# Performance work log

Hardware: AMD Instinct MI355X
Metric: run time of the kernel (lower is better)

Reference implementation:

```python
import jax, jax.numpy as jnp
import numpy as np

B, S, D = 4, 2048, 1024
E, K, H = 8, 2, 4096


def setup_inputs() -> dict:
    key = jax.random.key(0)
    ks = jax.random.split(key, 8)
    sd = 1.0 / np.sqrt(D)
    sh = 1.0 / np.sqrt(H)
    x = jax.random.normal(ks[0], (B, S, D), dtype=jnp.float32)
    gate_w = jax.random.normal(ks[1], (D, E), dtype=jnp.float32) * sd
    gate_b = jnp.zeros((E,), dtype=jnp.float32)
    w1 = jax.random.normal(ks[2], (E, D, H), dtype=jnp.float32) * sd
    b1 = jnp.zeros((E, H), dtype=jnp.float32)
    w2 = jax.random.normal(ks[3], (E, H, D), dtype=jnp.float32) * sh
    b2 = jnp.zeros((E, D), dtype=jnp.float32)
    return {"x": x, "gate_w": gate_w, "gate_b": gate_b,
            "w1": w1, "b1": b1, "w2": w2, "b2": b2}


def reference(x, gate_w, gate_b, w1, b1, w2, b2):
    # gate logits [B,S,E]
    logits = jnp.einsum('bsd,de->bse', x, gate_w) + gate_b
    # top-k over experts, softmax over the k selected (dim=2), in float32
    weights, selected = jax.lax.top_k(logits, K)            # [B,S,K]
    weights = jax.nn.softmax(weights.astype(jnp.float32), axis=-1).astype(x.dtype)
    out = jnp.zeros_like(x)
    for i in range(E):
        # per-token combine weight for expert i (0 if not routed here)
        w_i = jnp.sum(jnp.where(selected == i, weights, 0.0), axis=-1)  # [B,S]
        h = jax.nn.gelu(jnp.einsum('bsd,dh->bsh', x, w1[i]) + b1[i])    # [B,S,H]
        y = jnp.einsum('bsh,hd->bsd', h, w2[i]) + b2[i]                  # [B,S,D]
        out = out + w_i[..., None] * y
    return out
```

## Files before the change

### kernel.cpp

```cpp
#include <hip/hip_runtime.h>
#include <hip/hip_bf16.h>
#include <stdint.h>

#define T_TOK 8192
#define D_DIM 1024
#define E_NUM 8
#define H_DIM 4096
#define NPAD 144
#define PPX (NPAD / 8)
#define GATEB 2048
#define TRB 4096

typedef short bf16x8 __attribute__((ext_vector_type(8)));
typedef float f32x4 __attribute__((ext_vector_type(4)));
typedef unsigned short usv8 __attribute__((ext_vector_type(8)));

#define AS1 __attribute__((address_space(1)))
#define AS3 __attribute__((address_space(3)))

__device__ __forceinline__ unsigned short f2b(float f) {
  union { float f; uint32_t u; } v; v.f = f;
  uint32_t r = (v.u + 0x7fffu + ((v.u >> 16) & 1u)) >> 16;
  return (unsigned short)r;
}

__device__ __forceinline__ float gelu_tanh(float x) {
  float u = 0.7978845608028654f * (x + 0.044715f * x * x * x);
  u = fminf(fmaxf(u, -15.f), 15.f);
  float e = __expf(2.f * u);
  float t = (e - 1.f) / (e + 1.f);
  return 0.5f * x * (1.f + t);
}

__device__ __forceinline__ void gload_lds16(const void* g, void* l) {
  __builtin_amdgcn_global_load_lds((const AS1 uint32_t*)g, (AS3 uint32_t*)l, 16, 0, 0);
}

__global__ __launch_bounds__(256) void moe_prep(const float* __restrict__ x,
                                                const float* __restrict__ gw,
                                                const float* __restrict__ gb,
                                                const float* __restrict__ w1,
                                                const float* __restrict__ w2,
                                                const float* __restrict__ b2,
                                                unsigned short* __restrict__ xb,
                                                unsigned short* __restrict__ w1t,
                                                unsigned short* __restrict__ w2t,
                                                int2* __restrict__ sel,
                                                float2* __restrict__ wts,
                                                int* __restrict__ meta,
                                                float* __restrict__ out) {
  __shared__ unsigned short tile[64][260];
  int z = blockIdx.x;
  if (z >= GATEB) {
    int z2 = z - GATEB;
    int e = (z2 >> 8) & 7;
    int bx = z2 & 255;
    const float* in; unsigned short* outp; int R, C, ry, cy;
    if (z2 < TRB / 2) { in = w1 + (size_t)e * D_DIM * H_DIM; outp = w1t + (size_t)e * D_DIM * H_DIM;
                        R = D_DIM; C = H_DIM; ry = bx >> 6; cy = bx & 63; }
    else              { in = w2 + (size_t)e * H_DIM * D_DIM; outp = w2t + (size_t)e * H_DIM * D_DIM;
                        R = H_DIM; C = D_DIM; ry = bx >> 4; cy = bx & 15; }
    int r0 = ry * 256, c0 = cy * 64;
    int t = threadIdx.x;
    int sc = (t & 15) * 4;
    int srb = (t >> 4) * 4;
#pragma unroll
    for (int it = 0; it < 4; ++it) {
      int sr = srb + it * 64;
      float4 v0 = *(const float4*)(in + (size_t)(r0 + sr + 0) * C + c0 + sc);
      float4 v1 = *(const float4*)(in + (size_t)(r0 + sr + 1) * C + c0 + sc);
      float4 v2 = *(const float4*)(in + (size_t)(r0 + sr + 2) * C + c0 + sc);
      float4 v3 = *(const float4*)(in + (size_t)(r0 + sr + 3) * C + c0 + sc);
      ushort4 o;
      o.x = f2b(v0.x); o.y = f2b(v1.x); o.z = f2b(v2.x); o.w = f2b(v3.x);
      *(ushort4*)&tile[sc + 0][sr] = o;
      o.x = f2b(v0.y); o.y = f2b(v1.y); o.z = f2b(v2.y); o.w = f2b(v3.y);
      *(ushort4*)&tile[sc + 1][sr] = o;
      o.x = f2b(v0.z); o.y = f2b(v1.z); o.z = f2b(v2.z); o.w = f2b(v3.z);
      *(ushort4*)&tile[sc + 2][sr] = o;
      o.x = f2b(v0.w); o.y = f2b(v1.w); o.z = f2b(v2.w); o.w = f2b(v3.w);
      *(ushort4*)&tile[sc + 3][sr] = o;
    }
    __syncthreads();
    int wv = t >> 6, lane = t & 63;
    int rowHalf = lane >> 5, el = (lane & 31) * 8;
#pragma unroll
    for (int it = 0; it < 8; ++it) {
      int orow = wv * 16 + it * 2 + rowHalf;
      usv8 o = *(const usv8*)&tile[orow][el];
      *(usv8*)(outp + (size_t)(c0 + orow) * R + r0 + el) = o;
    }
    return;
  }
  int lane = threadIdx.x & 63;
  int t = z * 4 + (threadIdx.x >> 6);
  const float* xr = x + (size_t)t * D_DIM;
  unsigned short* xo = xb + (size_t)t * D_DIM;
  float acc[8];
#pragma unroll
  for (int e = 0; e < 8; e++) acc[e] = 0.f;
#pragma unroll
  for (int i = 0; i < 4; i++) {
    int d0 = lane * 4 + i * 256;
    float4 xv = *(const float4*)(xr + d0);
    ushort4 o;
    o.x = f2b(xv.x); o.y = f2b(xv.y); o.z = f2b(xv.z); o.w = f2b(xv.w);
    *(ushort4*)(xo + d0) = o;
    const float* gp = gw + (size_t)d0 * 8;
    float xs[4] = {xv.x, xv.y, xv.z, xv.w};
#pragma unroll
    for (int j = 0; j < 4; j++) {
#pragma unroll
      for (int e = 0; e < 8; e++) acc[e] += xs[j] * gp[j * 8 + e];
    }
  }
#pragma unroll
  for (int off = 32; off > 0; off >>= 1) {
#pragma unroll
    for (int e = 0; e < 8; e++) acc[e] += __shfl_xor(acc[e], off);
  }
  float lg[8];
#pragma unroll
  for (int e = 0; e < 8; e++) lg[e] = acc[e] + gb[e];
  int e0 = 0; float b0v = lg[0];
#pragma unroll
  for (int e = 1; e < 8; e++) if (lg[e] > b0v) { b0v = lg[e]; e0 = e; }
  int e1 = -1; float b1v = -1e30f;
#pragma unroll
  for (int e = 0; e < 8; e++) if (e != e0 && lg[e] > b1v) { b1v = lg[e]; e1 = e; }
  float d = __expf(b1v - b0v);
  float w0 = 1.f / (1.f + d), w1v = d / (1.f + d);
  if (lane == 0) {
    sel[t] = make_int2(e0, e1);
    wts[t] = make_float2(w0, w1v);
    atomicAdd(&meta[e0], 1);
    atomicAdd(&meta[e1], 1);
  }
  const float* ba = b2 + (size_t)e0 * D_DIM;
  const float* bb = b2 + (size_t)e1 * D_DIM;
  float* orow = out + (size_t)t * D_DIM;
#pragma unroll
  for (int k = 0; k < 4; k++) {
    int dd = lane * 4 + k * 256;
    float4 a = *(const float4*)(ba + dd);
    float4 b = *(const float4*)(bb + dd);
    float4 o;
    o.x = w0 * a.x + w1v * b.x;
    o.y = w0 * a.y + w1v * b.y;
    o.z = w0 * a.z + w1v * b.z;
    o.w = w0 * a.w + w1v * b.w;
    *(float4*)(orow + dd) = o;
  }
}

__global__ __launch_bounds__(256) void moe_scatter(const int2* __restrict__ sel,
                                                   const float2* __restrict__ wts,
                                                   int* __restrict__ meta,
                                                   int* __restrict__ token_id,
                                                   float* __restrict__ weightv) {
  int t = blockIdx.x * 256 + threadIdx.x;
  if (t >= T_TOK) return;
  int cnt[8];
#pragma unroll
  for (int e = 0; e < 8; e++) cnt[e] = meta[e];
  int2 s = sel[t];
  float2 w = wts[t];
  int o0 = 0, o1 = 0;
#pragma unroll
  for (int e = 0; e < 8; e++) {
    if (e < s.x) o0 += cnt[e];
    if (e < s.y) o1 += cnt[e];
  }
  int p0 = o0 + atomicAdd(&meta[20 + s.x], 1); token_id[p0] = t; weightv[p0] = w.x;
  int p1 = o1 + atomicAdd(&meta[20 + s.y], 1); token_id[p1] = t; weightv[p1] = w.y;
}

__device__ __forceinline__ bool panel_decode(const int* __restrict__ meta, int wi,
                                             int& e, int& m0, int& seg, int& ne) {
  int acc = 0, pre = 0;
  e = -1;
#pragma unroll
  for (int k = 0; k < 8; k++) {
    int ck = meta[k];
    int nb = (ck + 127) >> 7;
    if (wi >= acc && wi < acc + nb) { e = k; m0 = (wi - acc) << 7; seg = pre; ne = ck; }
    acc += nb; pre += ck;
  }
  return e >= 0;
}


__global__ __launch_bounds__(256, 4) void moe_gemm1(const unsigned short* __restrict__ xb,
                                                    const unsigned short* __restrict__ w1t,
                                                    const float* __restrict__ b1,
                                                    const int* __restrict__ meta,
                                                    const int* __restrict__ token_id,
                                                    unsigned short* __restrict__ hbuf) {
  int b = blockIdx.x;
  int c = b & 7, u = b >> 3;
  int n = u & 31, ps = u >> 5;
  int e, m0, seg, ne;
  if (!panel_decode(meta, c * PPX + ps, e, m0, seg, ne)) return;
  int n0 = n * 128;
  const unsigned short* wB = w1t + (size_t)e * H_DIM * D_DIM;

  __shared__ unsigned short As[2][4096];
  __shared__ unsigned short Bs[2][4096];

  int tid = threadIdx.x, lane = tid & 63, wv = tid >> 6;
  const unsigned short* aptr[2];
  const unsigned short* bptr[2];
#pragma unroll
  for (int q = 0; q < 2; q++) {
    int chunk = tid + q * 256;
    int row = chunk >> 2;
    int ko = ((chunk & 3) ^ ((chunk >> 3) & 3)) * 8;
    int gi = m0 + row; if (gi >= ne) gi = m0;
    int tok = token_id[seg + gi];
    aptr[q] = xb + (size_t)tok * D_DIM + ko;
    bptr[q] = wB + (size_t)(n0 + row) * D_DIM + ko;
  }
  auto stage = [&](int buf, int kt) {
#pragma unroll
    for (int q = 0; q < 2; q++) {
      gload_lds16(aptr[q] + kt * 32, &As[buf][(wv + 4 * q) * 512]);
      gload_lds16(bptr[q] + kt * 32, &Bs[buf][(wv + 4 * q) * 512]);
    }
  };

  f32x4 acc[4][4] = {};
  int wr = wv >> 1, wc = wv & 1;
  int sswz = ((lane >> 4) ^ ((lane >> 1) & 3)) * 8;
  int abase = (wr * 64 + (lane & 15)) * 32 + sswz;
  int bbase = (wc * 64 + (lane & 15)) * 32 + sswz;

  stage(0, 0);
  __syncthreads();
  const int nk = D_DIM / 32;
  for (int kt = 0; kt < nk; ++kt) {
    int cur = kt & 1;
    if (kt + 1 < nk) stage(cur ^ 1, kt + 1);
    bf16x8 af[4], bfr[4];
#pragma unroll
    for (int m = 0; m < 4; m++) af[m] = *(const bf16x8*)&As[cur][abase + m * 512];
#pragma unroll
    for (int nn = 0; nn < 4; nn++) bfr[nn] = *(const bf16x8*)&Bs[cur][bbase + nn * 512];
#pragma unroll
    for (int m = 0; m < 4; m++)
#pragma unroll
      for (int nn = 0; nn < 4; nn++)
        acc[m][nn] = __builtin_amdgcn_mfma_f32_16x16x32_bf16(af[m], bfr[nn], acc[m][nn], 0, 0, 0);
    __syncthreads();
  }

  int rbase = wr * 64 + (lane >> 4) * 4;
  int cbase = n0 + wc * 64 + (lane & 15);
  const float* b1e = b1 + (size_t)e * H_DIM + cbase;
  float bv[4];
#pragma unroll
  for (int nn = 0; nn < 4; nn++) bv[nn] = b1e[nn * 16];
#pragma unroll
  for (int m = 0; m < 4; m++) {
#pragma unroll
    for (int j = 0; j < 4; j++) {
      int gi = m0 + rbase + m * 16 + j;
      if (gi < ne) {
        unsigned short* hrow = hbuf + (size_t)(seg + gi) * H_DIM + cbase;
#pragma unroll
        for (int nn = 0; nn < 4; nn++) {
          float v = acc[m][nn][j] + bv[nn];
          hrow[nn * 16] = f2b(gelu_tanh(v));
        }
      }
    }
  }
}

__global__ __launch_bounds__(256, 4) void moe_gemm2(const unsigned short* __restrict__ hbuf,
                                                    const unsigned short* __restrict__ w2t,
                                                    const int* __restrict__ meta,
                                                    const int* __restrict__ token_id,
                                                    const float* __restrict__ weightv,
                                                    float* __restrict__ out) {
  int b = blockIdx.x;
  int c = b & 7, u = b >> 3;
  int n = u & 7, ks = (u >> 3) & 1, ps = u >> 4;
  int e, m0, seg, ne;
  if (!panel_decode(meta, c * PPX + ps, e, m0, seg, ne)) return;
  int n0 = n * 128;
  int kbase = ks * 2048;
  const unsigned short* wB = w2t + (size_t)e * D_DIM * H_DIM;

  __shared__ unsigned short As[2][4096];
  __shared__ unsigned short Bs[2][4096];

  int tid = threadIdx.x, lane = tid & 63, wv = tid >> 6;
  const unsigned short* aptr[2];
  const unsigned short* bptr[2];
#pragma unroll
  for (int q = 0; q < 2; q++) {
    int chunk = tid + q * 256;
    int row = chunk >> 2;
    int ko = ((chunk & 3) ^ ((chunk >> 3) & 3)) * 8;
    int gi = m0 + row; if (gi >= ne) gi = m0;
    aptr[q] = hbuf + (size_t)(seg + gi) * H_DIM + kbase + ko;
    bptr[q] = wB + (size_t)(n0 + row) * H_DIM + kbase + ko;
  }
  auto stage = [&](int buf, int kt) {
#pragma unroll
    for (int q = 0; q < 2; q++) {
      gload_lds16(aptr[q] + kt * 32, &As[buf][(wv + 4 * q) * 512]);
      gload_lds16(bptr[q] + kt * 32, &Bs[buf][(wv + 4 * q) * 512]);
    }
  };

  f32x4 acc[4][4] = {};
  int wr = wv >> 1, wc = wv & 1;
  int sswz = ((lane >> 4) ^ ((lane >> 1) & 3)) * 8;
  int abase = (wr * 64 + (lane & 15)) * 32 + sswz;
  int bbase = (wc * 64 + (lane & 15)) * 32 + sswz;

  stage(0, 0);
  __syncthreads();
  const int nk = 2048 / 32;
  for (int kt = 0; kt < nk; ++kt) {
    int cur = kt & 1;
    if (kt + 1 < nk) stage(cur ^ 1, kt + 1);
    bf16x8 af[4], bfr[4];
#pragma unroll
    for (int m = 0; m < 4; m++) af[m] = *(const bf16x8*)&As[cur][abase + m * 512];
#pragma unroll
    for (int nn = 0; nn < 4; nn++) bfr[nn] = *(const bf16x8*)&Bs[cur][bbase + nn * 512];
#pragma unroll
    for (int m = 0; m < 4; m++)
#pragma unroll
      for (int nn = 0; nn < 4; nn++)
        acc[m][nn] = __builtin_amdgcn_mfma_f32_16x16x32_bf16(af[m], bfr[nn], acc[m][nn], 0, 0, 0);
    __syncthreads();
  }

  int rbase = wr * 64 + (lane >> 4) * 4;
  int cbase = n0 + wc * 64 + (lane & 15);
#pragma unroll
  for (int m = 0; m < 4; m++) {
#pragma unroll
    for (int j = 0; j < 4; j++) {
      int gi = m0 + rbase + m * 16 + j;
      if (gi < ne) {
        int p = seg + gi;
        int tok = token_id[p];
        float wt = weightv[p];
        float* orow = out + (size_t)tok * D_DIM + cbase;
#pragma unroll
        for (int nn = 0; nn < 4; nn++)
          atomicAdd(&orow[nn * 16], wt * acc[m][nn][j]);
      }
    }
  }
}

extern "C" void kernel_launch(void* const* d_in, const int* in_sizes, int n_in,
                              void* d_out, int out_size, void* d_ws, size_t ws_size,
                              hipStream_t stream) {
  const float* x      = (const float*)d_in[0];
  const float* gate_w = (const float*)d_in[1];
  const float* gate_b = (const float*)d_in[2];
  const float* w1     = (const float*)d_in[3];
  const float* b1     = (const float*)d_in[4];
  const float* w2     = (const float*)d_in[5];
  const float* b2     = (const float*)d_in[6];
  float* out = (float*)d_out;

  uint8_t* ws = (uint8_t*)d_ws;
  unsigned short* hbuf = (unsigned short*)(ws);
  unsigned short* xb   = (unsigned short*)(ws + 134217728ull);
  unsigned short* w1t  = (unsigned short*)(ws + 150994944ull);
  unsigned short* w2t  = (unsigned short*)(ws + 218103808ull);
  int*    token_id = (int*)  (ws + 285212672ull);
  float*  weightv  = (float*)(ws + 285278208ull);
  float2* wts      = (float2*)(ws + 285343744ull);
  int2*   sel      = (int2*) (ws + 285409280ull);
  int*    meta     = (int*)  (ws + 285474816ull);

  hipMemsetAsync(meta, 0, 128, stream);

  moe_prep<<<dim3(GATEB + TRB), 256, 0, stream>>>(
      x, gate_w, gate_b, w1, w2, b2, xb, w1t, w2t, sel, wts, meta, out);
  moe_scatter<<<dim3(T_TOK / 256), 256, 0, stream>>>(sel, wts, meta, token_id, weightv);

  moe_gemm1<<<dim3(NPAD * 32), 256, 0, stream>>>(xb, w1t, b1, meta, token_id, hbuf);
  moe_gemm2<<<dim3(NPAD * 16), 256, 0, stream>>>(hbuf, w2t, meta, token_id, weightv, out);
}
```

Measured before the change: 795.9 us.

## Move w2 transpose into gemm1 launch to overlap with expert GEMM

Splits the weight transpose work so only w1 is converted in the prep kernel. The w2 fp32-to-bf16 transpose now runs as extra leading blocks in the gemm1 launch, sharing its LDS buffer (sized to fit the 64x260 tile). The aim is to shorten the prep kernel's critical path and overlap w2 conversion with the first GEMM's compute. In exchange, gemm1's shared memory allocation grows, which may reduce occupancy, and the transpose blocks compete with GEMM blocks for bandwidth and CUs.

```diff
diff --git a/kernel.cpp b/kernel.cpp
--- a/kernel.cpp
+++ b/kernel.cpp
@@ -9,7 +9,8 @@
 #define NPAD 144
 #define PPX (NPAD / 8)
 #define GATEB 2048
-#define TRB 4096
+#define TRB1 2048
+#define TRB2 2048
 
 typedef short bf16x8 __attribute__((ext_vector_type(8)));
 typedef float f32x4 __attribute__((ext_vector_type(4)));
@@ -36,15 +37,47 @@
   __builtin_amdgcn_global_load_lds((const AS1 uint32_t*)g, (AS3 uint32_t*)l, 16, 0, 0);
 }
 
+__device__ __forceinline__ void transpose_tile(const float* __restrict__ in,
+                                               unsigned short* __restrict__ outp,
+                                               int R, int C, int r0, int c0,
+                                               unsigned short (*tile)[260], int t) {
+  int sc = (t & 15) * 4;
+  int srb = (t >> 4) * 4;
+#pragma unroll
+  for (int it = 0; it < 4; ++it) {
+    int sr = srb + it * 64;
+    float4 v0 = *(const float4*)(in + (size_t)(r0 + sr + 0) * C + c0 + sc);
+    float4 v1 = *(const float4*)(in + (size_t)(r0 + sr + 1) * C + c0 + sc);
+    float4 v2 = *(const float4*)(in + (size_t)(r0 + sr + 2) * C + c0 + sc);
+    float4 v3 = *(const float4*)(in + (size_t)(r0 + sr + 3) * C + c0 + sc);
+    ushort4 o;
+    o.x = f2b(v0.x); o.y = f2b(v1.x); o.z = f2b(v2.x); o.w = f2b(v3.x);
+    *(ushort4*)&tile[sc + 0][sr] = o;
+    o.x = f2b(v0.y); o.y = f2b(v1.y); o.z = f2b(v2.y); o.w = f2b(v3.y);
+    *(ushort4*)&tile[sc + 1][sr] = o;
+    o.x = f2b(v0.z); o.y = f2b(v1.z); o.z = f2b(v2.z); o.w = f2b(v3.z);
+    *(ushort4*)&tile[sc + 2][sr] = o;
+    o.x = f2b(v0.w); o.y = f2b(v1.w); o.z = f2b(v2.w); o.w = f2b(v3.w);
+    *(ushort4*)&tile[sc + 3][sr] = o;
+  }
+  __syncthreads();
+  int wv = t >> 6, lane = t & 63;
+  int rowHalf = lane >> 5, el = (lane & 31) * 8;
+#pragma unroll
+  for (int it = 0; it < 8; ++it) {
+    int orow = wv * 16 + it * 2 + rowHalf;
+    usv8 o = *(const usv8*)&tile[orow][el];
+    *(usv8*)(outp + (size_t)(c0 + orow) * R + r0 + el) = o;
+  }
+}
+
 __global__ __launch_bounds__(256) void moe_prep(const float* __restrict__ x,
                                                 const float* __restrict__ gw,
                                                 const float* __restrict__ gb,
                                                 const float* __restrict__ w1,
-                                                const float* __restrict__ w2,
                                                 const float* __restrict__ b2,
                                                 unsigned short* __restrict__ xb,
                                                 unsigned short* __restrict__ w1t,
-                                                unsigned short* __restrict__ w2t,
                                                 int2* __restrict__ sel,
                                                 float2* __restrict__ wts,
                                                 int* __restrict__ meta,
@@ -53,43 +86,9 @@
   int z = blockIdx.x;
   if (z >= GATEB) {
     int z2 = z - GATEB;
-    int e = (z2 >> 8) & 7;
-    int bx = z2 & 255;
-    const float* in; unsigned short* outp; int R, C, ry, cy;
-    if (z2 < TRB / 2) { in = w1 + (size_t)e * D_DIM * H_DIM; outp = w1t + (size_t)e * D_DIM * H_DIM;
-                        R = D_DIM; C = H_DIM; ry = bx >> 6; cy = bx & 63; }
-    else              { in = w2 + (size_t)e * H_DIM * D_DIM; outp = w2t + (size_t)e * H_DIM * D_DIM;
-                        R = H_DIM; C = D_DIM; ry = bx >> 4; cy = bx & 15; }
-    int r0 = ry * 256, c0 = cy * 64;
-    int t = threadIdx.x;
-    int sc = (t & 15) * 4;
-    int srb = (t >> 4) * 4;
-#pragma unroll
-    for (int it = 0; it < 4; ++it) {
-      int sr = srb + it * 64;
-      float4 v0 = *(const float4*)(in + (size_t)(r0 + sr + 0) * C + c0 + sc);
-      float4 v1 = *(const float4*)(in + (size_t)(r0 + sr + 1) * C + c0 + sc);
-      float4 v2 = *(const float4*)(in + (size_t)(r0 + sr + 2) * C + c0 + sc);
-      float4 v3 = *(const float4*)(in + (size_t)(r0 + sr + 3) * C + c0 + sc);
-      ushort4 o;
-      o.x = f2b(v0.x); o.y = f2b(v1.x); o.z = f2b(v2.x); o.w = f2b(v3.x);
-      *(ushort4*)&tile[sc + 0][sr] = o;
-      o.x = f2b(v0.y); o.y = f2b(v1.y); o.z = f2b(v2.y); o.w = f2b(v3.y);
-      *(ushort4*)&tile[sc + 1][sr] = o;
-      o.x = f2b(v0.z); o.y = f2b(v1.z); o.z = f2b(v2.z); o.w = f2b(v3.z);
-      *(ushort4*)&tile[sc + 2][sr] = o;
-      o.x = f2b(v0.w); o.y = f2b(v1.w); o.z = f2b(v2.w); o.w = f2b(v3.w);
-      *(ushort4*)&tile[sc + 3][sr] = o;
-    }
-    __syncthreads();
-    int wv = t >> 6, lane = t & 63;
-    int rowHalf = lane >> 5, el = (lane & 31) * 8;
-#pragma unroll
-    for (int it = 0; it < 8; ++it) {
-      int orow = wv * 16 + it * 2 + rowHalf;
-      usv8 o = *(const usv8*)&tile[orow][el];
-      *(usv8*)(outp + (size_t)(c0 + orow) * R + r0 + el) = o;
-    }
+    int e = z2 >> 8, bx = z2 & 255;
+    transpose_tile(w1 + (size_t)e * D_DIM * H_DIM, w1t + (size_t)e * D_DIM * H_DIM,
+                   D_DIM, H_DIM, (bx >> 6) * 256, (bx & 63) * 64, tile, threadIdx.x);
     return;
   }
   int lane = threadIdx.x & 63;
@@ -189,14 +188,24 @@
   return e >= 0;
 }
 
-
 __global__ __launch_bounds__(256, 4) void moe_gemm1(const unsigned short* __restrict__ xb,
                                                     const unsigned short* __restrict__ w1t,
                                                     const float* __restrict__ b1,
+                                                    const float* __restrict__ w2,
+                                                    unsigned short* __restrict__ w2t,
                                                     const int* __restrict__ meta,
                                                     const int* __restrict__ token_id,
                                                     unsigned short* __restrict__ hbuf) {
-  int b = blockIdx.x;
+  __shared__ unsigned short SH[16640];
+  int z = blockIdx.x;
+  if (z < TRB2) {
+    int e = z >> 8, bx = z & 255;
+    transpose_tile(w2 + (size_t)e * H_DIM * D_DIM, w2t + (size_t)e * H_DIM * D_DIM,
+                   H_DIM, D_DIM, (bx >> 4) * 256, (bx & 15) * 64,
+                   (unsigned short (*)[260])SH, threadIdx.x);
+    return;
+  }
+  int b = z - TRB2;
   int c = b & 7, u = b >> 3;
   int n = u & 31, ps = u >> 5;
   int e, m0, seg, ne;
@@ -204,8 +213,8 @@
   int n0 = n * 128;
   const unsigned short* wB = w1t + (size_t)e * H_DIM * D_DIM;
 
-  __shared__ unsigned short As[2][4096];
-  __shared__ unsigned short Bs[2][4096];
+  unsigned short (*As)[4096] = (unsigned short (*)[4096])SH;
+  unsigned short (*Bs)[4096] = (unsigned short (*)[4096])(SH + 8192);
 
   int tid = threadIdx.x, lane = tid & 63, wv = tid >> 6;
   const unsigned short* aptr[2];
@@ -384,10 +393,11 @@
 
   hipMemsetAsync(meta, 0, 128, stream);
 
-  moe_prep<<<dim3(GATEB + TRB), 256, 0, stream>>>(
-      x, gate_w, gate_b, w1, w2, b2, xb, w1t, w2t, sel, wts, meta, out);
+  moe_prep<<<dim3(GATEB + TRB1), 256, 0, stream>>>(
+      x, gate_w, gate_b, w1, b2, xb, w1t, sel, wts, meta, out);
   moe_scatter<<<dim3(T_TOK / 256), 256, 0, stream>>>(sel, wts, meta, token_id, weightv);
 
-  moe_gemm1<<<dim3(NPAD * 32), 256, 0, stream>>>(xb, w1t, b1, meta, token_id, hbuf);
+  moe_gemm1<<<dim3(TRB2 + NPAD * 32), 256, 0, stream>>>(
+      xb, w1t, b1, w2, w2t, meta, token_id, hbuf);
   moe_gemm2<<<dim3(NPAD * 16), 256, 0, stream>>>(hbuf, w2t, meta, token_id, weightv, out);
 }
```

Result: no change. 793.3 us (-0.3%).
